# Optimization experiments

Measured on AMD Instinct MI355X. Metric: run time of the kernel, lower is better.

The kernel has to match this reference:

```python
import jax, jax.numpy as jnp
import numpy as np

B, T, D, H = 4, 2048, 768, 12
DH = D // H  # 64
SCALE = float(DH) ** 0.5  # NOTE: original code MULTIPLIES by sqrt(d_head)


def setup_inputs() -> dict:
    key = jax.random.key(0)
    k1, k2, k3 = jax.random.split(key, 3)
    x = jax.random.normal(k1, (B, T, D), dtype=jnp.float32)
    w_qkv = jax.random.normal(k2, (3 * D, D), dtype=jnp.float32) * (D ** -0.5)
    w_out = jax.random.normal(k3, (D, D), dtype=jnp.float32) * (D ** -0.5)
    return {"x": x, "w_qkv": w_qkv, "w_out": w_out}


def reference(x, w_qkv, w_out):
    b, t, d = x.shape
    # qkv_layer: Linear(d, 3d, bias=False) -> x @ W.T
    qkv = jnp.einsum('btd,ed->bte', x, w_qkv)  # [b, t, 3d]
    # rearrange 'b t (d k h) -> k b h t d' with k=3, h=H: split as (DH, 3, H)
    qkv = qkv.reshape(b, t, DH, 3, H)
    qkv = jnp.transpose(qkv, (3, 0, 4, 1, 2))  # [3, b, h, t, dh]
    q, k, v = qkv[0], qkv[1], qkv[2]
    # energy multiplied (faithfully) by sqrt(d_head)
    energy = jnp.einsum('bhid,bhjd->bhij', q, k) * SCALE
    attn = jax.nn.softmax(energy, axis=-1)
    o = jnp.einsum('bhij,bhjd->bhid', attn, v)  # [b, h, t, dh]
    # rearrange 'b h t d -> b t (h d)'
    o = jnp.transpose(o, (0, 2, 1, 3)).reshape(b, t, d)
    return jnp.einsum('btd,ed->bte', o, w_out)
```

## Files before the change

kernel.cpp:

```cpp
#include <hip/hip_runtime.h>
#include <hip/hip_bf16.h>
#include <cstdint>
#include <cstddef>

#define Bsz 4
#define Tsz 2048
#define Dsz 768
#define Hsz 12
#define DHsz 64
#define Msz (Bsz * Tsz)

typedef __attribute__((ext_vector_type(8))) short short8;
typedef __attribute__((ext_vector_type(4))) float floatx4;

__device__ __forceinline__ unsigned short f2bf(float f) {
  union { float f; unsigned u; } v; v.f = f;
  unsigned u = v.u;
  unsigned r = u + 0x7fffu + ((u >> 16) & 1u);
  return (unsigned short)(r >> 16);
}
__device__ __forceinline__ float bf2f(unsigned short h) {
  union { unsigned u; float f; } v; v.u = ((unsigned)h) << 16; return v.f;
}
__device__ __forceinline__ unsigned pk_bf2(float a, float b) {
  union { __hip_bfloat162 b2; unsigned u; } cv;
  cv.b2 = __float22bfloat162_rn(make_float2(a, b));
  return cv.u;
}

__global__ void split_x(const float* __restrict__ src,
                        unsigned short* __restrict__ hi,
                        unsigned short* __restrict__ lo) {
  int i = (blockIdx.x * blockDim.x + threadIdx.x) * 4;
  float4 v = *reinterpret_cast<const float4*>(src + i);
  ushort4 h, l;
  h.x = f2bf(v.x); l.x = f2bf(v.x - bf2f(h.x));
  h.y = f2bf(v.y); l.y = f2bf(v.y - bf2f(h.y));
  h.z = f2bf(v.z); l.z = f2bf(v.z - bf2f(h.z));
  h.w = f2bf(v.w); l.w = f2bf(v.w - bf2f(h.w));
  *reinterpret_cast<ushort4*>(hi + i) = h;
  *reinterpret_cast<ushort4*>(lo + i) = l;
}

__global__ void split_w(const float* __restrict__ src,
                        unsigned short* __restrict__ hi,
                        unsigned short* __restrict__ lo) {
  int i = (blockIdx.x * blockDim.x + threadIdx.x) * 4;
  int rp = i / Dsz, c = i % Dsz;
  int kk = rp / Dsz;
  int rem = rp - kk * Dsz;
  int h = rem >> 6, d = rem & 63;
  const float* s = src + (size_t)(d * 36 + kk * 12 + h) * Dsz + c;
  float4 v = *reinterpret_cast<const float4*>(s);
  ushort4 hh, ll;
  hh.x = f2bf(v.x); ll.x = f2bf(v.x - bf2f(hh.x));
  hh.y = f2bf(v.y); ll.y = f2bf(v.y - bf2f(hh.y));
  hh.z = f2bf(v.z); ll.z = f2bf(v.z - bf2f(hh.z));
  hh.w = f2bf(v.w); ll.w = f2bf(v.w - bf2f(hh.w));
  *reinterpret_cast<ushort4*>(hi + i) = hh;
  *reinterpret_cast<ushort4*>(lo + i) = ll;
}

__global__ void cvt_f32_bf16(const float* __restrict__ src,
                             unsigned short* __restrict__ dst, int n) {
  int i = (blockIdx.x * blockDim.x + threadIdx.x) * 4;
  int stride = gridDim.x * blockDim.x * 4;
  for (; i < n; i += stride) {
    float4 v = *reinterpret_cast<const float4*>(src + i);
    ushort4 o;
    o.x = f2bf(v.x); o.y = f2bf(v.y); o.z = f2bf(v.z); o.w = f2bf(v.w);
    *reinterpret_cast<ushort4*>(dst + i) = o;
  }
}

__launch_bounds__(256)
__global__ void gemm_qkv(const unsigned short* __restrict__ xh,
                         const unsigned short* __restrict__ xl,
                         const unsigned short* __restrict__ wh,
                         const unsigned short* __restrict__ wl,
                         unsigned short* __restrict__ Qhp,
                         unsigned short* __restrict__ Qlp,
                         unsigned short* __restrict__ Khp,
                         unsigned short* __restrict__ Klp,
                         unsigned short* __restrict__ Vtp) {
  __shared__ unsigned short Ah[64][72], Al[64][72];
  __shared__ unsigned short Bh[64][72], Bl[64][72];
  const int mt = blockIdx.x;
  const int nblk = blockIdx.y;
  const int kk = nblk / 12;
  const int h  = nblk % 12;
  const int tid = threadIdx.x;
  const int w = tid >> 6, lane = tid & 63, l16 = lane & 15, quad = lane >> 4;
  const int srow = tid >> 2;
  const int scol = (tid & 3) * 16;

  floatx4 acc[4];
#pragma unroll
  for (int i = 0; i < 4; ++i) acc[i] = (floatx4){0.f, 0.f, 0.f, 0.f};

  const size_t aoff = (size_t)(mt * 64 + srow) * Dsz + scol;
  const size_t boff = (size_t)(kk * Dsz + h * 64 + srow) * Dsz + scol;

  for (int kc = 0; kc < Dsz; kc += 64) {
    __syncthreads();
    *reinterpret_cast<short8*>(&Ah[srow][scol])     = *reinterpret_cast<const short8*>(xh + aoff + kc);
    *reinterpret_cast<short8*>(&Ah[srow][scol + 8]) = *reinterpret_cast<const short8*>(xh + aoff + kc + 8);
    *reinterpret_cast<short8*>(&Bh[srow][scol])     = *reinterpret_cast<const short8*>(wh + boff + kc);
    *reinterpret_cast<short8*>(&Bh[srow][scol + 8]) = *reinterpret_cast<const short8*>(wh + boff + kc + 8);
    if (kk != 2) {
      *reinterpret_cast<short8*>(&Al[srow][scol])     = *reinterpret_cast<const short8*>(xl + aoff + kc);
      *reinterpret_cast<short8*>(&Al[srow][scol + 8]) = *reinterpret_cast<const short8*>(xl + aoff + kc + 8);
      *reinterpret_cast<short8*>(&Bl[srow][scol])     = *reinterpret_cast<const short8*>(wl + boff + kc);
      *reinterpret_cast<short8*>(&Bl[srow][scol + 8]) = *reinterpret_cast<const short8*>(wl + boff + kc + 8);
    }
    __syncthreads();
#pragma unroll
    for (int s = 0; s < 2; ++s) {
      short8 ah = *reinterpret_cast<const short8*>(&Ah[w * 16 + l16][s * 32 + quad * 8]);
#pragma unroll
      for (int nt = 0; nt < 4; ++nt) {
        short8 bh = *reinterpret_cast<const short8*>(&Bh[nt * 16 + l16][s * 32 + quad * 8]);
        acc[nt] = __builtin_amdgcn_mfma_f32_16x16x32_bf16(ah, bh, acc[nt], 0, 0, 0);
      }
      if (kk != 2) {
        short8 al = *reinterpret_cast<const short8*>(&Al[w * 16 + l16][s * 32 + quad * 8]);
#pragma unroll
        for (int nt = 0; nt < 4; ++nt) {
          short8 bl = *reinterpret_cast<const short8*>(&Bl[nt * 16 + l16][s * 32 + quad * 8]);
          short8 bh = *reinterpret_cast<const short8*>(&Bh[nt * 16 + l16][s * 32 + quad * 8]);
          acc[nt] = __builtin_amdgcn_mfma_f32_16x16x32_bf16(ah, bl, acc[nt], 0, 0, 0);
          acc[nt] = __builtin_amdgcn_mfma_f32_16x16x32_bf16(al, bh, acc[nt], 0, 0, 0);
        }
      }
    }
  }
  const int mbase = mt * 64 + w * 16 + quad * 4;
  const int b = mbase >> 11;
  const size_t hoff = (size_t)(b * Hsz + h) * Tsz * DHsz;
  const int t0 = mbase & (Tsz - 1);
  if (kk == 2) {
    unsigned short* dst = Vtp + hoff;
#pragma unroll
    for (int nt = 0; nt < 4; ++nt) {
      int d = nt * 16 + l16;
      uint2 pk;
      pk.x = pk_bf2(acc[nt][0], acc[nt][1]);
      pk.y = pk_bf2(acc[nt][2], acc[nt][3]);
      *reinterpret_cast<uint2*>(&dst[(size_t)d * Tsz + t0]) = pk;
    }
  } else {
    const float sc = (kk == 0) ? 8.0f : 1.0f;
    unsigned short* dh_ = ((kk == 0) ? Qhp : Khp) + hoff;
    unsigned short* dl_ = ((kk == 0) ? Qlp : Klp) + hoff;
#pragma unroll
    for (int nt = 0; nt < 4; ++nt) {
      int d = nt * 16 + l16;
#pragma unroll
      for (int r = 0; r < 4; ++r) {
        float v = acc[nt][r] * sc;
        unsigned short hv = f2bf(v);
        dh_[(size_t)(t0 + r) * DHsz + d] = hv;
        dl_[(size_t)(t0 + r) * DHsz + d] = f2bf(v - bf2f(hv));
      }
    }
  }
}

__launch_bounds__(256, 3)
__global__ void attn(const unsigned short* __restrict__ Qhp,
                     const unsigned short* __restrict__ Qlp,
                     const unsigned short* __restrict__ Khp,
                     const unsigned short* __restrict__ Klp,
                     const unsigned short* __restrict__ Vtp,
                     unsigned short* __restrict__ Ob) {
  __shared__ unsigned short Ksh[64][72], Ksl[64][72], Vs[64][72];
  __shared__ unsigned short plT[4][2][16][72];
  const int bid = blockIdx.x;
  const int xcd = bid & 7, slot = bid >> 3;
  const int bh = xcd * 6 + (slot >> 4);
  const int qt = slot & 15;
  const int tid = threadIdx.x;
  const int w = tid >> 6, lane = tid & 63, l16 = lane & 15, quad = lane >> 4;
  const size_t hoff = (size_t)bh * Tsz * DHsz;
  const unsigned short* Kh = Khp + hoff;
  const unsigned short* Kl = Klp + hoff;
  const unsigned short* Vt = Vtp + hoff;

  const int strow = tid >> 3;
  const int stcol = (tid & 7) * 8;

  short8 qh[2][2], ql[2][2];
#pragma unroll
  for (int mt = 0; mt < 2; ++mt) {
    const size_t qoff = hoff + (size_t)(qt * 128 + w * 32 + mt * 16 + l16) * DHsz + quad * 8;
    qh[mt][0] = *reinterpret_cast<const short8*>(Qhp + qoff);
    qh[mt][1] = *reinterpret_cast<const short8*>(Qhp + qoff + 32);
    ql[mt][0] = *reinterpret_cast<const short8*>(Qlp + qoff);
    ql[mt][1] = *reinterpret_cast<const short8*>(Qlp + qoff + 32);
  }

  floatx4 Of[2][4];
#pragma unroll
  for (int mt = 0; mt < 2; ++mt)
#pragma unroll
    for (int nt = 0; nt < 4; ++nt) Of[mt][nt] = (floatx4){0.f, 0.f, 0.f, 0.f};
  float m_i[2] = {-1e30f, -1e30f};
  float l_i[2] = {0.f, 0.f};

  short8 rKh[2], rKl[2], rV[2];
#pragma unroll
  for (int p = 0; p < 2; ++p) {
    rKh[p] = *reinterpret_cast<const short8*>(Kh + (size_t)(strow + p * 32) * DHsz + stcol);
    rKl[p] = *reinterpret_cast<const short8*>(Kl + (size_t)(strow + p * 32) * DHsz + stcol);
    rV[p]  = *reinterpret_cast<const short8*>(Vt + (size_t)(strow + p * 32) * Tsz + stcol);
  }

  for (int kt = 0; kt < Tsz; kt += 64) {
    __syncthreads();
#pragma unroll
    for (int p = 0; p < 2; ++p) {
      *reinterpret_cast<short8*>(&Ksh[strow + p * 32][stcol]) = rKh[p];
      *reinterpret_cast<short8*>(&Ksl[strow + p * 32][stcol]) = rKl[p];
      *reinterpret_cast<short8*>(&Vs[strow + p * 32][stcol])  = rV[p];
    }
    __syncthreads();
    const int ktn = kt + 64;
    if (ktn < Tsz) {
#pragma unroll
      for (int p = 0; p < 2; ++p) {
        rKh[p] = *reinterpret_cast<const short8*>(Kh + (size_t)(ktn + strow + p * 32) * DHsz + stcol);
        rKl[p] = *reinterpret_cast<const short8*>(Kl + (size_t)(ktn + strow + p * 32) * DHsz + stcol);
        rV[p]  = *reinterpret_cast<const short8*>(Vt + (size_t)(strow + p * 32) * Tsz + ktn + stcol);
      }
    }

    floatx4 S[2][4];
#pragma unroll
    for (int mt = 0; mt < 2; ++mt)
#pragma unroll
      for (int nt = 0; nt < 4; ++nt) S[mt][nt] = (floatx4){0.f, 0.f, 0.f, 0.f};
#pragma unroll
    for (int s = 0; s < 2; ++s) {
#pragma unroll
      for (int nt = 0; nt < 4; ++nt) {
        short8 kf_h = *reinterpret_cast<const short8*>(&Ksh[nt * 16 + l16][s * 32 + quad * 8]);
        short8 kf_l = *reinterpret_cast<const short8*>(&Ksl[nt * 16 + l16][s * 32 + quad * 8]);
        S[0][nt] = __builtin_amdgcn_mfma_f32_16x16x32_bf16(kf_h, qh[0][s], S[0][nt], 0, 0, 0);
        S[0][nt] = __builtin_amdgcn_mfma_f32_16x16x32_bf16(kf_l, qh[0][s], S[0][nt], 0, 0, 0);
        S[0][nt] = __builtin_amdgcn_mfma_f32_16x16x32_bf16(kf_h, ql[0][s], S[0][nt], 0, 0, 0);
        S[1][nt] = __builtin_amdgcn_mfma_f32_16x16x32_bf16(kf_h, qh[1][s], S[1][nt], 0, 0, 0);
        S[1][nt] = __builtin_amdgcn_mfma_f32_16x16x32_bf16(kf_l, qh[1][s], S[1][nt], 0, 0, 0);
        S[1][nt] = __builtin_amdgcn_mfma_f32_16x16x32_bf16(kf_h, ql[1][s], S[1][nt], 0, 0, 0);
      }
    }

#pragma unroll
    for (int mt = 0; mt < 2; ++mt) {
      float mx = -1e30f;
#pragma unroll
      for (int nt = 0; nt < 4; ++nt)
#pragma unroll
        for (int r = 0; r < 4; ++r) mx = fmaxf(mx, S[mt][nt][r]);
      mx = fmaxf(mx, __shfl_xor(mx, 16));
      mx = fmaxf(mx, __shfl_xor(mx, 32));
      float mnew = fmaxf(m_i[mt], mx);
      float alpha = __expf(m_i[mt] - mnew);
      m_i[mt] = mnew;
      float ls = 0.f;
#pragma unroll
      for (int nt = 0; nt < 4; ++nt) {
        float p0 = __expf(S[mt][nt][0] - mnew);
        float p1 = __expf(S[mt][nt][1] - mnew);
        float p2 = __expf(S[mt][nt][2] - mnew);
        float p3 = __expf(S[mt][nt][3] - mnew);
        ls += (p0 + p1) + (p2 + p3);
        uint2 pk;
        pk.x = pk_bf2(p0, p1);
        pk.y = pk_bf2(p2, p3);
        *reinterpret_cast<uint2*>(&plT[w][mt][l16][nt * 16 + quad * 4]) = pk;
      }
      l_i[mt] = l_i[mt] * alpha + ls;
#pragma unroll
      for (int nt = 0; nt < 4; ++nt) {
        Of[mt][nt][0] *= alpha; Of[mt][nt][1] *= alpha;
        Of[mt][nt][2] *= alpha; Of[mt][nt][3] *= alpha;
      }
    }

    short8 pf[2][2];
#pragma unroll
    for (int s = 0; s < 2; ++s) {
      pf[0][s] = *reinterpret_cast<const short8*>(&plT[w][0][l16][s * 32 + quad * 8]);
      pf[1][s] = *reinterpret_cast<const short8*>(&plT[w][1][l16][s * 32 + quad * 8]);
    }
#pragma unroll
    for (int nt = 0; nt < 4; ++nt) {
#pragma unroll
      for (int s = 0; s < 2; ++s) {
        short8 vf = *reinterpret_cast<const short8*>(&Vs[nt * 16 + l16][s * 32 + quad * 8]);
        Of[0][nt] = __builtin_amdgcn_mfma_f32_16x16x32_bf16(vf, pf[0][s], Of[0][nt], 0, 0, 0);
        Of[1][nt] = __builtin_amdgcn_mfma_f32_16x16x32_bf16(vf, pf[1][s], Of[1][nt], 0, 0, 0);
      }
    }
  }

  const int b = bh / Hsz, h = bh % Hsz;
#pragma unroll
  for (int mt = 0; mt < 2; ++mt) {
    float ls = l_i[mt];
    ls += __shfl_xor(ls, 16);
    ls += __shfl_xor(ls, 32);
    float inv = 1.0f / ls;
    int t = qt * 128 + w * 32 + mt * 16 + l16;
    unsigned short* orow = Ob + (size_t)(b * Tsz + t) * Dsz + h * DHsz;
#pragma unroll
    for (int nt = 0; nt < 4; ++nt) {
      uint2 pk;
      pk.x = pk_bf2(Of[mt][nt][0] * inv, Of[mt][nt][1] * inv);
      pk.y = pk_bf2(Of[mt][nt][2] * inv, Of[mt][nt][3] * inv);
      *reinterpret_cast<uint2*>(&orow[nt * 16 + quad * 4]) = pk;
    }
  }
}

__launch_bounds__(256)
__global__ void gemm_out(const unsigned short* __restrict__ ob,
                         const unsigned short* __restrict__ wb,
                         float* __restrict__ out) {
  __shared__ unsigned short As[64][72];
  __shared__ unsigned short Bs[64][72];
  const int mt = blockIdx.x;
  const int n0 = blockIdx.y * 64;
  const int tid = threadIdx.x;
  const int w = tid >> 6, lane = tid & 63, l16 = lane & 15, quad = lane >> 4;
  const int srow = tid >> 2;
  const int scol = (tid & 3) * 16;

  floatx4 acc[4];
#pragma unroll
  for (int i = 0; i < 4; ++i) acc[i] = (floatx4){0.f, 0.f, 0.f, 0.f};

  const unsigned short* gA = ob + (size_t)(mt * 64 + srow) * Dsz + scol;
  const unsigned short* gB = wb + (size_t)(n0 + srow) * Dsz + scol;

  for (int kc = 0; kc < Dsz; kc += 64) {
    __syncthreads();
    *reinterpret_cast<short8*>(&As[srow][scol])     = *reinterpret_cast<const short8*>(gA + kc);
    *reinterpret_cast<short8*>(&As[srow][scol + 8]) = *reinterpret_cast<const short8*>(gA + kc + 8);
    *reinterpret_cast<short8*>(&Bs[srow][scol])     = *reinterpret_cast<const short8*>(gB + kc);
    *reinterpret_cast<short8*>(&Bs[srow][scol + 8]) = *reinterpret_cast<const short8*>(gB + kc + 8);
    __syncthreads();
#pragma unroll
    for (int s = 0; s < 2; ++s) {
      short8 a = *reinterpret_cast<const short8*>(&As[w * 16 + l16][s * 32 + quad * 8]);
#pragma unroll
      for (int nt = 0; nt < 4; ++nt) {
        short8 b = *reinterpret_cast<const short8*>(&Bs[nt * 16 + l16][s * 32 + quad * 8]);
        acc[nt] = __builtin_amdgcn_mfma_f32_16x16x32_bf16(a, b, acc[nt], 0, 0, 0);
      }
    }
  }
  const int mbase = mt * 64 + w * 16 + quad * 4;
#pragma unroll
  for (int nt = 0; nt < 4; ++nt) {
    int n = n0 + nt * 16 + l16;
#pragma unroll
    for (int r = 0; r < 4; ++r) {
      out[(size_t)(mbase + r) * Dsz + n] = acc[nt][r];
    }
  }
}

extern "C" void kernel_launch(void* const* d_in, const int* in_sizes, int n_in,
                              void* d_out, int out_size, void* d_ws, size_t ws_size,
                              hipStream_t stream) {
  const float* x     = (const float*)d_in[0];
  const float* w_qkv = (const float*)d_in[1];
  const float* w_out = (const float*)d_in[2];
  float* out = (float*)d_out;

  unsigned short* ws = (unsigned short*)d_ws;
  const size_t nX  = (size_t)Msz * Dsz;
  const size_t nWq = (size_t)3 * Dsz * Dsz;
  const size_t nWo = (size_t)Dsz * Dsz;
  const size_t nHd = (size_t)Bsz * Hsz * Tsz * DHsz;

  unsigned short* xh  = ws;
  unsigned short* xl  = xh + nX;
  unsigned short* wh  = xl + nX;
  unsigned short* wl  = wh + nWq;
  unsigned short* wob = wl + nWq;
  unsigned short* Qhp = wob + nWo;
  unsigned short* Qlp = Qhp + nHd;
  unsigned short* Khp = Qlp + nHd;
  unsigned short* Klp = Khp + nHd;
  unsigned short* Vtp = Klp + nHd;
  unsigned short* Ob  = xh;

  split_x<<<nX / 4 / 256, 256, 0, stream>>>(x, xh, xl);
  split_w<<<nWq / 4 / 256, 256, 0, stream>>>(w_qkv, wh, wl);
  cvt_f32_bf16<<<256, 256, 0, stream>>>(w_out, wob, (int)nWo);
  gemm_qkv<<<dim3(128, 36), 256, 0, stream>>>(xh, xl, wh, wl, Qhp, Qlp, Khp, Klp, Vtp);
  attn<<<768, 256, 0, stream>>>(Qhp, Qlp, Khp, Klp, Vtp, Ob);
  gemm_out<<<dim3(128, 12), 256, 0, stream>>>(Ob, wob, out);
}
```

Before: 322.6 us.

## Double GEMM M-tile to 128 and read attention K/V directly from global

The QKV and output GEMMs now compute 128x64 tiles per block, reusing each B fragment across two M sub-tiles and halving grid size, with unpadded shared arrays. The attention kernel drops its shared-memory staging and register prefetch of K and V, and instead loads MFMA fragments directly from global memory each iteration. This removes block barriers and LDS traffic in attention but relies on caches to serve the repeated per-wave loads, loses the software prefetch, and the unpadded LDS rows may introduce bank conflicts.

```diff
diff --git a/kernel.cpp b/kernel.cpp
--- a/kernel.cpp
+++ b/kernel.cpp
@@ -73,7 +73,7 @@
   }
 }
 
-__launch_bounds__(256)
+__launch_bounds__(256, 3)
 __global__ void gemm_qkv(const unsigned short* __restrict__ xh,
                          const unsigned short* __restrict__ xl,
                          const unsigned short* __restrict__ wh,
@@ -83,9 +83,9 @@
                          unsigned short* __restrict__ Khp,
                          unsigned short* __restrict__ Klp,
                          unsigned short* __restrict__ Vtp) {
-  __shared__ unsigned short Ah[64][72], Al[64][72];
-  __shared__ unsigned short Bh[64][72], Bl[64][72];
-  const int mt = blockIdx.x;
+  __shared__ unsigned short Ah[128][64], Al[128][64];
+  __shared__ unsigned short Bh[64][64],  Bl[64][64];
+  const int mt128 = blockIdx.x;
   const int nblk = blockIdx.y;
   const int kk = nblk / 12;
   const int h  = nblk % 12;
@@ -94,73 +94,90 @@
   const int srow = tid >> 2;
   const int scol = (tid & 3) * 16;
 
-  floatx4 acc[4];
-#pragma unroll
-  for (int i = 0; i < 4; ++i) acc[i] = (floatx4){0.f, 0.f, 0.f, 0.f};
-
-  const size_t aoff = (size_t)(mt * 64 + srow) * Dsz + scol;
+  floatx4 acc[2][4];
+#pragma unroll
+  for (int mt = 0; mt < 2; ++mt)
+#pragma unroll
+    for (int nt = 0; nt < 4; ++nt) acc[mt][nt] = (floatx4){0.f, 0.f, 0.f, 0.f};
+
+  const size_t aoff = (size_t)(mt128 * 128 + srow) * Dsz + scol;
   const size_t boff = (size_t)(kk * Dsz + h * 64 + srow) * Dsz + scol;
 
   for (int kc = 0; kc < Dsz; kc += 64) {
     __syncthreads();
-    *reinterpret_cast<short8*>(&Ah[srow][scol])     = *reinterpret_cast<const short8*>(xh + aoff + kc);
-    *reinterpret_cast<short8*>(&Ah[srow][scol + 8]) = *reinterpret_cast<const short8*>(xh + aoff + kc + 8);
-    *reinterpret_cast<short8*>(&Bh[srow][scol])     = *reinterpret_cast<const short8*>(wh + boff + kc);
-    *reinterpret_cast<short8*>(&Bh[srow][scol + 8]) = *reinterpret_cast<const short8*>(wh + boff + kc + 8);
+    *reinterpret_cast<short8*>(&Ah[srow][scol])          = *reinterpret_cast<const short8*>(xh + aoff + kc);
+    *reinterpret_cast<short8*>(&Ah[srow][scol + 8])      = *reinterpret_cast<const short8*>(xh + aoff + kc + 8);
+    *reinterpret_cast<short8*>(&Ah[srow + 64][scol])     = *reinterpret_cast<const short8*>(xh + aoff + (size_t)64 * Dsz + kc);
+    *reinterpret_cast<short8*>(&Ah[srow + 64][scol + 8]) = *reinterpret_cast<const short8*>(xh + aoff + (size_t)64 * Dsz + kc + 8);
+    *reinterpret_cast<short8*>(&Bh[srow][scol])          = *reinterpret_cast<const short8*>(wh + boff + kc);
+    *reinterpret_cast<short8*>(&Bh[srow][scol + 8])      = *reinterpret_cast<const short8*>(wh + boff + kc + 8);
     if (kk != 2) {
-      *reinterpret_cast<short8*>(&Al[srow][scol])     = *reinterpret_cast<const short8*>(xl + aoff + kc);
-      *reinterpret_cast<short8*>(&Al[srow][scol + 8]) = *reinterpret_cast<const short8*>(xl + aoff + kc + 8);
-      *reinterpret_cast<short8*>(&Bl[srow][scol])     = *reinterpret_cast<const short8*>(wl + boff + kc);
-      *reinterpret_cast<short8*>(&Bl[srow][scol + 8]) = *reinterpret_cast<const short8*>(wl + boff + kc + 8);
+      *reinterpret_cast<short8*>(&Al[srow][scol])          = *reinterpret_cast<const short8*>(xl + aoff + kc);
+      *reinterpret_cast<short8*>(&Al[srow][scol + 8])      = *reinterpret_cast<const short8*>(xl + aoff + kc + 8);
+      *reinterpret_cast<short8*>(&Al[srow + 64][scol])     = *reinterpret_cast<const short8*>(xl + aoff + (size_t)64 * Dsz + kc);
+      *reinterpret_cast<short8*>(&Al[srow + 64][scol + 8]) = *reinterpret_cast<const short8*>(xl + aoff + (size_t)64 * Dsz + kc + 8);
+      *reinterpret_cast<short8*>(&Bl[srow][scol])          = *reinterpret_cast<const short8*>(wl + boff + kc);
+      *reinterpret_cast<short8*>(&Bl[srow][scol + 8])      = *reinterpret_cast<const short8*>(wl + boff + kc + 8);
     }
     __syncthreads();
 #pragma unroll
     for (int s = 0; s < 2; ++s) {
-      short8 ah = *reinterpret_cast<const short8*>(&Ah[w * 16 + l16][s * 32 + quad * 8]);
+      short8 ah[2], al[2];
+#pragma unroll
+      for (int mt = 0; mt < 2; ++mt)
+        ah[mt] = *reinterpret_cast<const short8*>(&Ah[w * 32 + mt * 16 + l16][s * 32 + quad * 8]);
+      if (kk != 2) {
+#pragma unroll
+        for (int mt = 0; mt < 2; ++mt)
+          al[mt] = *reinterpret_cast<const short8*>(&Al[w * 32 + mt * 16 + l16][s * 32 + quad * 8]);
+      }
 #pragma unroll
       for (int nt = 0; nt < 4; ++nt) {
         short8 bh = *reinterpret_cast<const short8*>(&Bh[nt * 16 + l16][s * 32 + quad * 8]);
-        acc[nt] = __builtin_amdgcn_mfma_f32_16x16x32_bf16(ah, bh, acc[nt], 0, 0, 0);
-      }
-      if (kk != 2) {
-        short8 al = *reinterpret_cast<const short8*>(&Al[w * 16 + l16][s * 32 + quad * 8]);
-#pragma unroll
-        for (int nt = 0; nt < 4; ++nt) {
+#pragma unroll
+        for (int mt = 0; mt < 2; ++mt)
+          acc[mt][nt] = __builtin_amdgcn_mfma_f32_16x16x32_bf16(ah[mt], bh, acc[mt][nt], 0, 0, 0);
+        if (kk != 2) {
           short8 bl = *reinterpret_cast<const short8*>(&Bl[nt * 16 + l16][s * 32 + quad * 8]);
-          short8 bh = *reinterpret_cast<const short8*>(&Bh[nt * 16 + l16][s * 32 + quad * 8]);
-          acc[nt] = __builtin_amdgcn_mfma_f32_16x16x32_bf16(ah, bl, acc[nt], 0, 0, 0);
-          acc[nt] = __builtin_amdgcn_mfma_f32_16x16x32_bf16(al, bh, acc[nt], 0, 0, 0);
+#pragma unroll
+          for (int mt = 0; mt < 2; ++mt) {
+            acc[mt][nt] = __builtin_amdgcn_mfma_f32_16x16x32_bf16(ah[mt], bl, acc[mt][nt], 0, 0, 0);
+            acc[mt][nt] = __builtin_amdgcn_mfma_f32_16x16x32_bf16(al[mt], bh, acc[mt][nt], 0, 0, 0);
+          }
         }
       }
     }
   }
-  const int mbase = mt * 64 + w * 16 + quad * 4;
-  const int b = mbase >> 11;
-  const size_t hoff = (size_t)(b * Hsz + h) * Tsz * DHsz;
-  const int t0 = mbase & (Tsz - 1);
-  if (kk == 2) {
-    unsigned short* dst = Vtp + hoff;
-#pragma unroll
-    for (int nt = 0; nt < 4; ++nt) {
-      int d = nt * 16 + l16;
-      uint2 pk;
-      pk.x = pk_bf2(acc[nt][0], acc[nt][1]);
-      pk.y = pk_bf2(acc[nt][2], acc[nt][3]);
-      *reinterpret_cast<uint2*>(&dst[(size_t)d * Tsz + t0]) = pk;
-    }
-  } else {
-    const float sc = (kk == 0) ? 8.0f : 1.0f;
-    unsigned short* dh_ = ((kk == 0) ? Qhp : Khp) + hoff;
-    unsigned short* dl_ = ((kk == 0) ? Qlp : Klp) + hoff;
-#pragma unroll
-    for (int nt = 0; nt < 4; ++nt) {
-      int d = nt * 16 + l16;
-#pragma unroll
-      for (int r = 0; r < 4; ++r) {
-        float v = acc[nt][r] * sc;
-        unsigned short hv = f2bf(v);
-        dh_[(size_t)(t0 + r) * DHsz + d] = hv;
-        dl_[(size_t)(t0 + r) * DHsz + d] = f2bf(v - bf2f(hv));
+#pragma unroll
+  for (int mt = 0; mt < 2; ++mt) {
+    const int mbase = mt128 * 128 + w * 32 + mt * 16 + quad * 4;
+    const int b = mbase >> 11;
+    const size_t hoff = (size_t)(b * Hsz + h) * Tsz * DHsz;
+    const int t0 = mbase & (Tsz - 1);
+    if (kk == 2) {
+      unsigned short* dst = Vtp + hoff;
+#pragma unroll
+      for (int nt = 0; nt < 4; ++nt) {
+        int d = nt * 16 + l16;
+        uint2 pk;
+        pk.x = pk_bf2(acc[mt][nt][0], acc[mt][nt][1]);
+        pk.y = pk_bf2(acc[mt][nt][2], acc[mt][nt][3]);
+        *reinterpret_cast<uint2*>(&dst[(size_t)d * Tsz + t0]) = pk;
+      }
+    } else {
+      const float sc = (kk == 0) ? 8.0f : 1.0f;
+      unsigned short* dh_ = ((kk == 0) ? Qhp : Khp) + hoff;
+      unsigned short* dl_ = ((kk == 0) ? Qlp : Klp) + hoff;
+#pragma unroll
+      for (int nt = 0; nt < 4; ++nt) {
+        int d = nt * 16 + l16;
+#pragma unroll
+        for (int r = 0; r < 4; ++r) {
+          float v = acc[mt][nt][r] * sc;
+          unsigned short hv = f2bf(v);
+          dh_[(size_t)(t0 + r) * DHsz + d] = hv;
+          dl_[(size_t)(t0 + r) * DHsz + d] = f2bf(v - bf2f(hv));
+        }
       }
     }
   }
@@ -173,7 +190,6 @@
                      const unsigned short* __restrict__ Klp,
                      const unsigned short* __restrict__ Vtp,
                      unsigned short* __restrict__ Ob) {
-  __shared__ unsigned short Ksh[64][72], Ksl[64][72], Vs[64][72];
   __shared__ unsigned short plT[4][2][16][72];
   const int bid = blockIdx.x;
   const int xcd = bid & 7, slot = bid >> 3;
@@ -186,9 +202,6 @@
   const unsigned short* Kl = Klp + hoff;
   const unsigned short* Vt = Vtp + hoff;
 
-  const int strow = tid >> 3;
-  const int stcol = (tid & 7) * 8;
-
   short8 qh[2][2], ql[2][2];
 #pragma unroll
   for (int mt = 0; mt < 2; ++mt) {
@@ -207,33 +220,7 @@
   float m_i[2] = {-1e30f, -1e30f};
   float l_i[2] = {0.f, 0.f};
 
-  short8 rKh[2], rKl[2], rV[2];
-#pragma unroll
-  for (int p = 0; p < 2; ++p) {
-    rKh[p] = *reinterpret_cast<const short8*>(Kh + (size_t)(strow + p * 32) * DHsz + stcol);
-    rKl[p] = *reinterpret_cast<const short8*>(Kl + (size_t)(strow + p * 32) * DHsz + stcol);
-    rV[p]  = *reinterpret_cast<const short8*>(Vt + (size_t)(strow + p * 32) * Tsz + stcol);
-  }
-
   for (int kt = 0; kt < Tsz; kt += 64) {
-    __syncthreads();
-#pragma unroll
-    for (int p = 0; p < 2; ++p) {
-      *reinterpret_cast<short8*>(&Ksh[strow + p * 32][stcol]) = rKh[p];
-      *reinterpret_cast<short8*>(&Ksl[strow + p * 32][stcol]) = rKl[p];
-      *reinterpret_cast<short8*>(&Vs[strow + p * 32][stcol])  = rV[p];
-    }
-    __syncthreads();
-    const int ktn = kt + 64;
-    if (ktn < Tsz) {
-#pragma unroll
-      for (int p = 0; p < 2; ++p) {
-        rKh[p] = *reinterpret_cast<const short8*>(Kh + (size_t)(ktn + strow + p * 32) * DHsz + stcol);
-        rKl[p] = *reinterpret_cast<const short8*>(Kl + (size_t)(ktn + strow + p * 32) * DHsz + stcol);
-        rV[p]  = *reinterpret_cast<const short8*>(Vt + (size_t)(strow + p * 32) * Tsz + ktn + stcol);
-      }
-    }
-
     floatx4 S[2][4];
 #pragma unroll
     for (int mt = 0; mt < 2; ++mt)
@@ -243,8 +230,9 @@
     for (int s = 0; s < 2; ++s) {
 #pragma unroll
       for (int nt = 0; nt < 4; ++nt) {
-        short8 kf_h = *reinterpret_cast<const short8*>(&Ksh[nt * 16 + l16][s * 32 + quad * 8]);
-        short8 kf_l = *reinterpret_cast<const short8*>(&Ksl[nt * 16 + l16][s * 32 + quad * 8]);
+        const size_t koff = (size_t)(kt + nt * 16 + l16) * DHsz + s * 32 + quad * 8;
+        short8 kf_h = *reinterpret_cast<const short8*>(Kh + koff);
+        short8 kf_l = *reinterpret_cast<const short8*>(Kl + koff);
         S[0][nt] = __builtin_amdgcn_mfma_f32_16x16x32_bf16(kf_h, qh[0][s], S[0][nt], 0, 0, 0);
         S[0][nt] = __builtin_amdgcn_mfma_f32_16x16x32_bf16(kf_l, qh[0][s], S[0][nt], 0, 0, 0);
         S[0][nt] = __builtin_amdgcn_mfma_f32_16x16x32_bf16(kf_h, ql[0][s], S[0][nt], 0, 0, 0);
@@ -297,7 +285,8 @@
     for (int nt = 0; nt < 4; ++nt) {
 #pragma unroll
       for (int s = 0; s < 2; ++s) {
-        short8 vf = *reinterpret_cast<const short8*>(&Vs[nt * 16 + l16][s * 32 + quad * 8]);
+        short8 vf = *reinterpret_cast<const short8*>(
+            Vt + (size_t)(nt * 16 + l16) * Tsz + kt + s * 32 + quad * 8);
         Of[0][nt] = __builtin_amdgcn_mfma_f32_16x16x32_bf16(vf, pf[0][s], Of[0][nt], 0, 0, 0);
         Of[1][nt] = __builtin_amdgcn_mfma_f32_16x16x32_bf16(vf, pf[1][s], Of[1][nt], 0, 0, 0);
       }
@@ -323,50 +312,62 @@
   }
 }
 
-__launch_bounds__(256)
+__launch_bounds__(256, 3)
 __global__ void gemm_out(const unsigned short* __restrict__ ob,
                          const unsigned short* __restrict__ wb,
                          float* __restrict__ out) {
-  __shared__ unsigned short As[64][72];
-  __shared__ unsigned short Bs[64][72];
-  const int mt = blockIdx.x;
+  __shared__ unsigned short As[128][64];
+  __shared__ unsigned short Bs[64][64];
+  const int mt128 = blockIdx.x;
   const int n0 = blockIdx.y * 64;
   const int tid = threadIdx.x;
   const int w = tid >> 6, lane = tid & 63, l16 = lane & 15, quad = lane >> 4;
   const int srow = tid >> 2;
   const int scol = (tid & 3) * 16;
 
-  floatx4 acc[4];
-#pragma unroll
-  for (int i = 0; i < 4; ++i) acc[i] = (floatx4){0.f, 0.f, 0.f, 0.f};
-
-  const unsigned short* gA = ob + (size_t)(mt * 64 + srow) * Dsz + scol;
-  const unsigned short* gB = wb + (size_t)(n0 + srow) * Dsz + scol;
+  floatx4 acc[2][4];
+#pragma unroll
+  for (int mt = 0; mt < 2; ++mt)
+#pragma unroll
+    for (int nt = 0; nt < 4; ++nt) acc[mt][nt] = (floatx4){0.f, 0.f, 0.f, 0.f};
+
+  const size_t aoff = (size_t)(mt128 * 128 + srow) * Dsz + scol;
+  const size_t boff = (size_t)(n0 + srow) * Dsz + scol;
 
   for (int kc = 0; kc < Dsz; kc += 64) {
     __syncthreads();
-    *reinterpret_cast<short8*>(&As[srow][scol])     = *reinterpret_cast<const short8*>(gA + kc);
-    *reinterpret_cast<short8*>(&As[srow][scol + 8]) = *reinterpret_cast<const short8*>(gA + kc + 8);
-    *reinterpret_cast<short8*>(&Bs[srow][scol])     = *reinterpret_cast<const short8*>(gB + kc);
-    *reinterpret_cast<short8*>(&Bs[srow][scol + 8]) = *reinterpret_cast<const short8*>(gB + kc + 8);
+    *reinterpret_cast<short8*>(&As[srow][scol])          = *reinterpret_cast<const short8*>(ob + aoff + kc);
+    *reinterpret_cast<short8*>(&As[srow][scol + 8])      = *reinterpret_cast<const short8*>(ob + aoff + kc + 8);
+    *reinterpret_cast<short8*>(&As[srow + 64][scol])     = *reinterpret_cast<const short8*>(ob + aoff + (size_t)64 * Dsz + kc);
+    *reinterpret_cast<short8*>(&As[srow + 64][scol + 8]) = *reinterpret_cast<const short8*>(ob + aoff + (size_t)64 * Dsz + kc + 8);
+    *reinterpret_cast<short8*>(&Bs[srow][scol])          = *reinterpret_cast<const short8*>(wb + boff + kc);
+    *reinterpret_cast<short8*>(&Bs[srow][scol + 8])      = *reinterpret_cast<const short8*>(wb + boff + kc + 8);
     __syncthreads();
 #pragma unroll
     for (int s = 0; s < 2; ++s) {
-      short8 a = *reinterpret_cast<const short8*>(&As[w * 16 + l16][s * 32 + quad * 8]);
+      short8 a[2];
+#pragma unroll
+      for (int mt = 0; mt < 2; ++mt)
+        a[mt] = *reinterpret_cast<const short8*>(&As[w * 32 + mt * 16 + l16][s * 32 + quad * 8]);
 #pragma unroll
       for (int nt = 0; nt < 4; ++nt) {
         short8 b = *reinterpret_cast<const short8*>(&Bs[nt * 16 + l16][s * 32 + quad * 8]);
-        acc[nt] = __builtin_amdgcn_mfma_f32_16x16x32_bf16(a, b, acc[nt], 0, 0, 0);
-      }
-    }
-  }
-  const int mbase = mt * 64 + w * 16 + quad * 4;
-#pragma unroll
-  for (int nt = 0; nt < 4; ++nt) {
-    int n = n0 + nt * 16 + l16;
-#pragma unroll
-    for (int r = 0; r < 4; ++r) {
-      out[(size_t)(mbase + r) * Dsz + n] = acc[nt][r];
+#pragma unroll
+        for (int mt = 0; mt < 2; ++mt)
+          acc[mt][nt] = __builtin_amdgcn_mfma_f32_16x16x32_bf16(a[mt], b, acc[mt][nt], 0, 0, 0);
+      }
+    }
+  }
+#pragma unroll
+  for (int mt = 0; mt < 2; ++mt) {
+    const int mbase = mt128 * 128 + w * 32 + mt * 16 + quad * 4;
+#pragma unroll
+    for (int nt = 0; nt < 4; ++nt) {
+      int n = n0 + nt * 16 + l16;
+#pragma unroll
+      for (int r = 0; r < 4; ++r) {
+        out[(size_t)(mbase + r) * Dsz + n] = acc[mt][nt][r];
+      }
     }
   }
 }
@@ -400,7 +401,7 @@
   split_x<<<nX / 4 / 256, 256, 0, stream>>>(x, xh, xl);
   split_w<<<nWq / 4 / 256, 256, 0, stream>>>(w_qkv, wh, wl);
   cvt_f32_bf16<<<256, 256, 0, stream>>>(w_out, wob, (int)nWo);
-  gemm_qkv<<<dim3(128, 36), 256, 0, stream>>>(xh, xl, wh, wl, Qhp, Qlp, Khp, Klp, Vtp);
+  gemm_qkv<<<dim3(64, 36), 256, 0, stream>>>(xh, xl, wh, wl, Qhp, Qlp, Khp, Klp, Vtp);
   attn<<<768, 256, 0, stream>>>(Qhp, Qlp, Khp, Klp, Vtp, Ob);
-  gemm_out<<<dim3(128, 12), 256, 0, stream>>>(Ob, wob, out);
-}
+  gemm_out<<<dim3(64, 12), 256, 0, stream>>>(Ob, wob, out);
+}
```

Result: slower. 476.7 us (+47.7%).
